# Optimization experiments

Measured on AMD Instinct MI355X. Metric: run time of the kernel, lower is better.

Reference implementation:

```python
import jax, jax.numpy as jnp
import numpy as np

EPS = 1e-10
ENTROPY_COEF = 0.1
COLSUM_COEF = 1.0


def setup_inputs() -> dict:
    key = jax.random.key(0)
    k1, k2, k3 = jax.random.split(key, 3)
    H, T, B, S = 512, 50003, 32, 256
    colsum_threshold = 0.5
    return {
        "text_input": jax.random.randint(k1, (B, S), 0, T, dtype=jnp.int32),
        "init_logits": jnp.zeros((H,), dtype=jnp.float32),
        "transition_logits": jax.random.normal(k2, (H, H), dtype=jnp.float32) * 0.1,
        "emission_logits": jax.random.normal(k3, (H, T), dtype=jnp.float32) * 0.1,
        "colsum_threshold": colsum_threshold,
    }


def reference(text_input, init_logits, transition_logits, emission_logits, colsum_threshold):
    # softmax-normalized HMM parameters
    text_pi = jax.nn.softmax(init_logits, axis=0)              # [H]
    text_A = jax.nn.softmax(transition_logits, axis=1)         # [H,H]
    text_B = jax.nn.softmax(emission_logits, axis=1)           # [H,T]

    log_pi = jnp.log(text_pi + EPS)                            # [H]
    log_A = jnpp = jnp.log(text_A + EPS)                       # [H,H]
    log_B = jnp.log(text_B + EPS)                              # [H,T]

    # gather per-token emission log-probs: [B,S,H]
    log_B_obs = log_B.T[text_input]

    # t = 0
    log_alpha0 = log_pi[None, :] + log_B_obs[:, 0, :]          # [B,H]

    def step(log_alpha, obs_t):
        # logsumexp over source state i: [B,H(i),1] + [1,H(i),H(j)] -> [B,H(j)]
        trans = log_alpha[:, :, None] + log_A[None, :, :]
        new_alpha = jax.nn.logsumexp(trans, axis=1) + obs_t
        return new_alpha, None

    obs_rest = jnp.swapaxes(log_B_obs[:, 1:, :], 0, 1)         # [S-1,B,H]
    log_alpha_final, _ = jax.lax.scan(step, log_alpha0, obs_rest)

    log_likelihood = jax.nn.logsumexp(log_alpha_final, axis=1)  # [B]
    likelihood_loss = -jnp.mean(log_likelihood)

    transition_entropy = -jnp.sum(text_A * jnp.log(text_A + EPS), axis=1)
    transition_entropy_loss = jnp.mean(transition_entropy) * ENTROPY_COEF

    col_sums = jnp.sum(text_A, axis=0)
    colsum_reg = jnp.sum(jax.nn.relu(colsum_threshold - col_sums)) * COLSUM_COEF

    hmm_loss = likelihood_loss + transition_entropy_loss + colsum_reg
    return text_pi, text_A, text_B, hmm_loss
```

## Files before the change

### kernel.cpp

```cpp
#include <hip/hip_runtime.h>
#include <hip/hip_bf16.h>
#include <stdint.h>

#define HH 512
#define BB 32
#define SSEQ 256
#define TVOC 50003
#define EPSF 1e-10f
#define EMSCALE 96.0f
#define TOTLOG 2759.2459164008406f

typedef float f32x4 __attribute__((ext_vector_type(4)));
typedef int v8i __attribute__((ext_vector_type(8)));

__device__ __forceinline__ float wave_max(float v) {
#pragma unroll
  for (int off = 32; off; off >>= 1) v = fmaxf(v, __shfl_xor(v, off));
  return v;
}
__device__ __forceinline__ float wave_sum(float v) {
#pragma unroll
  for (int off = 32; off; off >>= 1) v += __shfl_xor(v, off);
  return v;
}

__global__ __launch_bounds__(512) void init_ws_kernel(float* ws) {
  if (threadIdx.x < 8) ws[threadIdx.x] = 0.0f;
  ws[8 + threadIdx.x] = 0.0f;
}

__global__ __launch_bounds__(512) void softmax_pi_kernel(
    const float* __restrict__ x, float* __restrict__ pi) {
  const int tid = threadIdx.x;
  const int wv = tid >> 6, ln = tid & 63;
  __shared__ float red[8];
  float v = x[tid];
  float m = wave_max(v);
  if (ln == 0) red[wv] = m;
  __syncthreads();
  float M = red[0];
#pragma unroll
  for (int i = 1; i < 8; ++i) M = fmaxf(M, red[i]);
  float e = __expf(v - M);
  float s = wave_sum(e);
  __syncthreads();
  if (ln == 0) red[wv] = s;
  __syncthreads();
  float S = 0.f;
#pragma unroll
  for (int i = 0; i < 8; ++i) S += red[i];
  pi[tid] = e / S;
}

__global__ __launch_bounds__(512) void softmaxA_kernel(
    const float* __restrict__ tl, float* __restrict__ outA,
    float* __restrict__ ws_ent) {
  const int r = blockIdx.x, tid = threadIdx.x;
  const int wv = tid >> 6, ln = tid & 63;
  __shared__ float red[8];
  float v = tl[(size_t)r * HH + tid];
  float m = wave_max(v);
  if (ln == 0) red[wv] = m;
  __syncthreads();
  float M = red[0];
#pragma unroll
  for (int i = 1; i < 8; ++i) M = fmaxf(M, red[i]);
  float e = __expf(v - M);
  float s = wave_sum(e);
  __syncthreads();
  if (ln == 0) red[wv] = s;
  __syncthreads();
  float S = 0.f;
#pragma unroll
  for (int i = 0; i < 8; ++i) S += red[i];
  float p = e / S;
  outA[(size_t)r * HH + tid] = p;
  float ent = -p * __logf(p + EPSF);
  ent = wave_sum(ent);
  __syncthreads();
  if (ln == 0) red[wv] = ent;
  __syncthreads();
  if (tid == 0) {
    float tot = 0.f;
#pragma unroll
    for (int i = 0; i < 8; ++i) tot += red[i];
    atomicAdd(ws_ent, tot);
  }
}

__global__ __launch_bounds__(512) void colsum_partial_kernel(
    const float* __restrict__ outA, float* __restrict__ col) {
  const int j = threadIdx.x;
  const int i0 = blockIdx.x * 64;
  float s = 0.f;
#pragma unroll 4
  for (int i = i0; i < i0 + 64; ++i) s += outA[(size_t)i * HH + j];
  atomicAdd(&col[j], s);
}

__global__ __launch_bounds__(1024) void softmaxB_gather_kernel(
    const float* __restrict__ el, float* __restrict__ outB,
    const int* __restrict__ tok, __hip_bfloat16* __restrict__ ems) {
  const int r = blockIdx.x, tid = threadIdx.x;
  const float* x = el + (size_t)r * TVOC;
  float* yo = outB + (size_t)r * TVOC;
  const int mis = (int)(((16u - ((unsigned)(uintptr_t)x & 15u)) & 15u) >> 2);
  const int body = (TVOC - mis) >> 2;
  const int tailoff = mis + body * 4;

  float m = -1e30f, s = 0.f;
  auto upd = [&m, &s](float v) {
    if (v > m) { s = s * __expf(m - v) + 1.f; m = v; }
    else       { s += __expf(v - m); }
  };
  if (tid < mis) upd(x[tid]);
  const float4* x4 = (const float4*)(x + mis);
  for (int i = tid; i < body; i += 1024) {
    float4 v = x4[i];
    upd(v.x); upd(v.y); upd(v.z); upd(v.w);
  }
  for (int i = tailoff + tid; i < TVOC; i += 1024) upd(x[i]);

#pragma unroll
  for (int off = 32; off; off >>= 1) {
    float om = __shfl_down(m, off), os = __shfl_down(s, off);
    float nm = fmaxf(m, om);
    s = s * __expf(m - nm) + os * __expf(om - nm);
    m = nm;
  }
  __shared__ float sm[16], ssv[16];
  __shared__ float bM, biZ;
  if ((tid & 63) == 0) { sm[tid >> 6] = m; ssv[tid >> 6] = s; }
  __syncthreads();
  if (tid == 0) {
    float M = sm[0], S = ssv[0];
#pragma unroll
    for (int w = 1; w < 16; ++w) {
      float nm = fmaxf(M, sm[w]);
      S = S * __expf(M - nm) + ssv[w] * __expf(sm[w] - nm);
      M = nm;
    }
    bM = M; biZ = 1.f / S;
  }
  __syncthreads();
  const float M = bM, iZ = biZ;
  if (tid < mis) yo[tid] = __expf(x[tid] - M) * iZ;
  float4* y4 = (float4*)(yo + mis);
  for (int i = tid; i < body; i += 1024) {
    float4 v = x4[i];
    float4 o;
    o.x = __expf(v.x - M) * iZ;
    o.y = __expf(v.y - M) * iZ;
    o.z = __expf(v.z - M) * iZ;
    o.w = __expf(v.w - M) * iZ;
    y4[i] = o;
  }
  for (int i = tailoff + tid; i < TVOC; i += 1024)
    yo[i] = __expf(x[i] - M) * iZ;

  const float gs = EMSCALE * iZ;
  for (int idx = tid; idx < BB * SSEQ; idx += 1024) {
    const int sq = idx >> 5, b = idx & 31;
    const int t = tok[b * SSEQ + sq];
    ems[((size_t)sq * HH + r) * BB + b] = __float2bfloat16(__expf(x[t] - M) * gs);
  }
}

__global__ __launch_bounds__(1024) void scan_kernel(
    const float* __restrict__ d_pi, const float* __restrict__ d_A,
    const __hip_bfloat16* __restrict__ ems, float* __restrict__ ws_negll) {
  const int h = blockIdx.x;
  const int tid = threadIdx.x;
  const int lane = tid & 63;
  const int wave = tid >> 6;
  const int l15 = lane & 15;
  const int quad = lane >> 4;

  __shared__ __align__(16) unsigned char alpha[2][16][528];
  __shared__ float wmax[16][17];
  __shared__ float wsum[16][17];
  __shared__ float ls[16];

  const unsigned short* emsu = (const unsigned short*)ems;

  v8i aF[2][4];
#pragma unroll
  for (int n = 0; n < 2; ++n) {
    const int jg = wave * 32 + n * 16 + l15;
#pragma unroll
    for (int c = 0; c < 4; ++c) {
#pragma unroll
      for (int g = 0; g < 8; ++g) {
        const int k0 = c * 128 + quad * 32 + g * 4;
        const float v0 = d_A[(size_t)(k0 + 0) * HH + jg] * 512.0f;
        const float v1 = d_A[(size_t)(k0 + 1) * HH + jg] * 512.0f;
        const float v2 = d_A[(size_t)(k0 + 2) * HH + jg] * 512.0f;
        const float v3 = d_A[(size_t)(k0 + 3) * HH + jg] * 512.0f;
        int wrd = 0;
        wrd = __builtin_amdgcn_cvt_pk_fp8_f32(v0, v1, wrd, false);
        wrd = __builtin_amdgcn_cvt_pk_fp8_f32(v2, v3, wrd, true);
        aF[n][c][g] = wrd;
      }
    }
  }

  {
    const int b = wave;
    const int j0 = lane * 8;
    float vals[8];
    float m = -1e30f;
#pragma unroll
    for (int u = 0; u < 8; ++u) {
      const float e = __bfloat162float(ems[(size_t)(j0 + u) * BB + h * 16 + b]);
      vals[u] = (d_pi[j0 + u] + EPSF) * e;
      m = fmaxf(m, vals[u]);
    }
    m = wave_max(m);
    if (lane == 0) ls[b] = __logf(m);
    const float r = 1.0f / m;
    int lo = 0, hi = 0;
    lo = __builtin_amdgcn_cvt_pk_fp8_f32(vals[0] * r, vals[1] * r, lo, false);
    lo = __builtin_amdgcn_cvt_pk_fp8_f32(vals[2] * r, vals[3] * r, lo, true);
    hi = __builtin_amdgcn_cvt_pk_fp8_f32(vals[4] * r, vals[5] * r, hi, false);
    hi = __builtin_amdgcn_cvt_pk_fp8_f32(vals[6] * r, vals[7] * r, hi, true);
    *(unsigned int*)&alpha[0][b][j0]     = (unsigned)lo;
    *(unsigned int*)&alpha[0][b][j0 + 4] = (unsigned)hi;
  }
  __syncthreads();

  unsigned short evr[2][4];
#pragma unroll
  for (int n = 0; n < 2; ++n)
#pragma unroll
    for (int rg = 0; rg < 4; ++rg) {
      const int j = wave * 32 + n * 16 + quad * 4 + rg;
      evr[n][rg] = emsu[((size_t)1 * HH + j) * BB + h * 16 + l15];
    }

#pragma unroll 1
  for (int t = 1; t < SSEQ; ++t) {
    const int cur = (t - 1) & 1, nxt = t & 1;

    float ev[2][4];
#pragma unroll
    for (int n = 0; n < 2; ++n)
#pragma unroll
      for (int rg = 0; rg < 4; ++rg) {
        const unsigned u = (unsigned)evr[n][rg] << 16;
        ev[n][rg] = __uint_as_float(u);
      }
    const int tp = (t + 1 < SSEQ) ? t + 1 : SSEQ - 1;
#pragma unroll
    for (int n = 0; n < 2; ++n)
#pragma unroll
      for (int rg = 0; rg < 4; ++rg) {
        const int j = wave * 32 + n * 16 + quad * 4 + rg;
        evr[n][rg] = emsu[((size_t)tp * HH + j) * BB + h * 16 + l15];
      }

    f32x4 acc0 = {0.f, 0.f, 0.f, 0.f}, acc1 = {0.f, 0.f, 0.f, 0.f};
#pragma unroll
    for (int c = 0; c < 4; ++c) {
      const unsigned char* ap = &alpha[cur][l15][c * 128 + quad * 32];
      const int4 lo = *(const int4*)ap;
      const int4 hi = *(const int4*)(ap + 16);
      v8i bf;
      bf[0] = lo.x; bf[1] = lo.y; bf[2] = lo.z; bf[3] = lo.w;
      bf[4] = hi.x; bf[5] = hi.y; bf[6] = hi.z; bf[7] = hi.w;
      acc0 = __builtin_amdgcn_mfma_scale_f32_16x16x128_f8f6f4(
          aF[0][c], bf, acc0, 0, 0, 0, 0x7F7F7F7F, 0, 0x7F7F7F7F);
      acc1 = __builtin_amdgcn_mfma_scale_f32_16x16x128_f8f6f4(
          aF[1][c], bf, acc1, 0, 0, 0, 0x7F7F7F7F, 0, 0x7F7F7F7F);
    }

    float y[2][4];
#pragma unroll
    for (int rg = 0; rg < 4; ++rg) {
      y[0][rg] = acc0[rg] * ev[0][rg];
      y[1][rg] = acc1[rg] * ev[1][rg];
    }

    float r = 1.0f;
    if ((t & 15) == 0) {
      float mm = -1e30f;
#pragma unroll
      for (int rg = 0; rg < 4; ++rg)
        mm = fmaxf(mm, fmaxf(y[0][rg], y[1][rg]));
      mm = fmaxf(mm, __shfl_xor(mm, 16));
      mm = fmaxf(mm, __shfl_xor(mm, 32));
      if (lane < 16) wmax[wave][lane] = mm;
      __syncthreads();
      float m = wmax[0][l15];
#pragma unroll
      for (int w = 1; w < 16; ++w) m = fmaxf(m, wmax[w][l15]);
      r = 1.0f / m;
      if (tid < 16) ls[tid] += __logf(m);
    }

#pragma unroll
    for (int n = 0; n < 2; ++n) {
      int d = 0;
      d = __builtin_amdgcn_cvt_pk_fp8_f32(y[n][0] * r, y[n][1] * r, d, false);
      d = __builtin_amdgcn_cvt_pk_fp8_f32(y[n][2] * r, y[n][3] * r, d, true);
      *(unsigned int*)&alpha[nxt][l15][wave * 32 + n * 16 + quad * 4] = (unsigned)d;
    }
    if (t == SSEQ - 1) {
      float s = (y[0][0] + y[0][1] + y[0][2] + y[0][3] +
                 y[1][0] + y[1][1] + y[1][2] + y[1][3]) * r;
      s += __shfl_xor(s, 16);
      s += __shfl_xor(s, 32);
      if (lane < 16) wsum[wave][lane] = s;
    }
    __syncthreads();
  }

  if (wave == 0 && lane < 16) {
    float s = 0.f;
#pragma unroll
    for (int w = 0; w < 16; ++w) s += wsum[w][lane];
    const float LL = __logf(s) + ls[lane] - TOTLOG;
    atomicAdd(ws_negll, -LL * (1.0f / 32.0f));
  }
}

__global__ __launch_bounds__(512) void finalize_kernel(
    const float* __restrict__ ws, const float* __restrict__ col,
    const float* __restrict__ thr, float* __restrict__ out_loss) {
  const int j = threadIdx.x;
  float v = fmaxf(thr[0] - col[j], 0.f);
  v = wave_sum(v);
  __shared__ float red[8];
  if ((j & 63) == 0) red[j >> 6] = v;
  __syncthreads();
  if (j == 0) {
    float creg = 0.f;
#pragma unroll
    for (int i = 0; i < 8; ++i) creg += red[i];
    out_loss[0] = ws[1] + ws[0] * (0.1f / 512.0f) + creg;
  }
}

extern "C" void kernel_launch(void* const* d_in, const int* in_sizes, int n_in,
                              void* d_out, int out_size, void* d_ws, size_t ws_size,
                              hipStream_t stream) {
  const int*   tok    = (const int*)d_in[0];
  const float* initl  = (const float*)d_in[1];
  const float* transl = (const float*)d_in[2];
  const float* eml    = (const float*)d_in[3];
  const float* thr    = (const float*)d_in[4];

  float* out      = (float*)d_out;
  float* out_pi   = out;
  float* out_A    = out + HH;
  float* out_B    = out + HH + (size_t)HH * HH;
  float* out_loss = out + HH + (size_t)HH * HH + (size_t)HH * TVOC;

  float* wsf = (float*)d_ws;
  float* col = wsf + 8;
  __hip_bfloat16* ems = (__hip_bfloat16*)((char*)d_ws + 4096);

  init_ws_kernel<<<1, 512, 0, stream>>>(wsf);
  softmax_pi_kernel<<<1, 512, 0, stream>>>(initl, out_pi);
  softmaxA_kernel<<<512, 512, 0, stream>>>(transl, out_A, wsf + 0);
  colsum_partial_kernel<<<8, 512, 0, stream>>>(out_A, col);
  softmaxB_gather_kernel<<<512, 1024, 0, stream>>>(eml, out_B, tok, ems);
  scan_kernel<<<2, 1024, 0, stream>>>(out_pi, out_A, ems, wsf + 1);
  finalize_kernel<<<1, 512, 0, stream>>>(wsf, col, thr, out_loss);
}
```

Measured before the change: 598.1 us.

## Halve scan block to 8 waves with 64 output columns each; widen colsum grid

The scan kernel now runs 512 threads (8 waves) per block, and each wave computes four 16-column MFMA tiles instead of two. This keeps twice as much of the fp8 transition matrix in registers per wave and halves the number of waves taking part in each per-step barrier. The aim is to cut barrier and cross-wave synchronisation cost on the serial 255-step recurrence, at the price of more work per wave and higher register pressure. Separately, the colsum kernel is split across 32 blocks of 16 rows instead of 8 blocks of 64.

```diff
diff --git a/kernel.cpp b/kernel.cpp
--- a/kernel.cpp
+++ b/kernel.cpp
@@ -91,10 +91,10 @@
 __global__ __launch_bounds__(512) void colsum_partial_kernel(
     const float* __restrict__ outA, float* __restrict__ col) {
   const int j = threadIdx.x;
-  const int i0 = blockIdx.x * 64;
+  const int i0 = blockIdx.x * 16;
   float s = 0.f;
 #pragma unroll 4
-  for (int i = i0; i < i0 + 64; ++i) s += outA[(size_t)i * HH + j];
+  for (int i = i0; i < i0 + 16; ++i) s += outA[(size_t)i * HH + j];
   atomicAdd(&col[j], s);
 }
 
@@ -166,7 +166,7 @@
   }
 }
 
-__global__ __launch_bounds__(1024) void scan_kernel(
+__global__ __launch_bounds__(512, 2) void scan_kernel(
     const float* __restrict__ d_pi, const float* __restrict__ d_A,
     const __hip_bfloat16* __restrict__ ems, float* __restrict__ ws_negll) {
   const int h = blockIdx.x;
@@ -177,16 +177,16 @@
   const int quad = lane >> 4;
 
   __shared__ __align__(16) unsigned char alpha[2][16][528];
-  __shared__ float wmax[16][17];
-  __shared__ float wsum[16][17];
+  __shared__ float wmax[8][17];
+  __shared__ float wsum[8][17];
   __shared__ float ls[16];
 
   const unsigned short* emsu = (const unsigned short*)ems;
 
-  v8i aF[2][4];
-#pragma unroll
-  for (int n = 0; n < 2; ++n) {
-    const int jg = wave * 32 + n * 16 + l15;
+  v8i aF[4][4];
+#pragma unroll
+  for (int n = 0; n < 4; ++n) {
+    const int jg = wave * 64 + n * 16 + l15;
 #pragma unroll
     for (int c = 0; c < 4; ++c) {
 #pragma unroll
@@ -205,35 +205,37 @@
   }
 
   {
-    const int b = wave;
-    const int j0 = lane * 8;
-    float vals[8];
+    const int b = wave * 2 + (lane >> 5);
+    const int lh = lane & 31;
+    const int j0 = lh * 16;
+    float vals[16];
     float m = -1e30f;
 #pragma unroll
-    for (int u = 0; u < 8; ++u) {
+    for (int u = 0; u < 16; ++u) {
       const float e = __bfloat162float(ems[(size_t)(j0 + u) * BB + h * 16 + b]);
       vals[u] = (d_pi[j0 + u] + EPSF) * e;
       m = fmaxf(m, vals[u]);
     }
-    m = wave_max(m);
-    if (lane == 0) ls[b] = __logf(m);
+#pragma unroll
+    for (int off = 16; off; off >>= 1) m = fmaxf(m, __shfl_xor(m, off));
+    if (lh == 0) ls[b] = __logf(m);
     const float r = 1.0f / m;
-    int lo = 0, hi = 0;
-    lo = __builtin_amdgcn_cvt_pk_fp8_f32(vals[0] * r, vals[1] * r, lo, false);
-    lo = __builtin_amdgcn_cvt_pk_fp8_f32(vals[2] * r, vals[3] * r, lo, true);
-    hi = __builtin_amdgcn_cvt_pk_fp8_f32(vals[4] * r, vals[5] * r, hi, false);
-    hi = __builtin_amdgcn_cvt_pk_fp8_f32(vals[6] * r, vals[7] * r, hi, true);
-    *(unsigned int*)&alpha[0][b][j0]     = (unsigned)lo;
-    *(unsigned int*)&alpha[0][b][j0 + 4] = (unsigned)hi;
-  }
-  __syncthreads();
-
-  unsigned short evr[2][4];
-#pragma unroll
-  for (int n = 0; n < 2; ++n)
+#pragma unroll
+    for (int d = 0; d < 4; ++d) {
+      int wrd = 0;
+      wrd = __builtin_amdgcn_cvt_pk_fp8_f32(vals[d*4+0] * r, vals[d*4+1] * r, wrd, false);
+      wrd = __builtin_amdgcn_cvt_pk_fp8_f32(vals[d*4+2] * r, vals[d*4+3] * r, wrd, true);
+      *(unsigned int*)&alpha[0][b][j0 + d * 4] = (unsigned)wrd;
+    }
+  }
+  __syncthreads();
+
+  unsigned short evr[4][4];
+#pragma unroll
+  for (int n = 0; n < 4; ++n)
 #pragma unroll
     for (int rg = 0; rg < 4; ++rg) {
-      const int j = wave * 32 + n * 16 + quad * 4 + rg;
+      const int j = wave * 64 + n * 16 + quad * 4 + rg;
       evr[n][rg] = emsu[((size_t)1 * HH + j) * BB + h * 16 + l15];
     }
 
@@ -241,24 +243,24 @@
   for (int t = 1; t < SSEQ; ++t) {
     const int cur = (t - 1) & 1, nxt = t & 1;
 
-    float ev[2][4];
-#pragma unroll
-    for (int n = 0; n < 2; ++n)
-#pragma unroll
-      for (int rg = 0; rg < 4; ++rg) {
-        const unsigned u = (unsigned)evr[n][rg] << 16;
-        ev[n][rg] = __uint_as_float(u);
-      }
+    float ev[4][4];
+#pragma unroll
+    for (int n = 0; n < 4; ++n)
+#pragma unroll
+      for (int rg = 0; rg < 4; ++rg)
+        ev[n][rg] = __uint_as_float((unsigned)evr[n][rg] << 16);
+
     const int tp = (t + 1 < SSEQ) ? t + 1 : SSEQ - 1;
-#pragma unroll
-    for (int n = 0; n < 2; ++n)
-#pragma unroll
-      for (int rg = 0; rg < 4; ++rg) {
-        const int j = wave * 32 + n * 16 + quad * 4 + rg;
-        evr[n][rg] = emsu[((size_t)tp * HH + j) * BB + h * 16 + l15];
-      }
-
-    f32x4 acc0 = {0.f, 0.f, 0.f, 0.f}, acc1 = {0.f, 0.f, 0.f, 0.f};
+    const unsigned short* ep =
+        emsu + ((size_t)tp * HH + wave * 64 + quad * 4) * BB + h * 16 + l15;
+#pragma unroll
+    for (int n = 0; n < 4; ++n)
+#pragma unroll
+      for (int rg = 0; rg < 4; ++rg)
+        evr[n][rg] = ep[(n * 16 + rg) * BB];
+
+    f32x4 acc[4] = {{0.f,0.f,0.f,0.f},{0.f,0.f,0.f,0.f},
+                    {0.f,0.f,0.f,0.f},{0.f,0.f,0.f,0.f}};
 #pragma unroll
     for (int c = 0; c < 4; ++c) {
       const unsigned char* ap = &alpha[cur][l15][c * 128 + quad * 32];
@@ -267,46 +269,50 @@
       v8i bf;
       bf[0] = lo.x; bf[1] = lo.y; bf[2] = lo.z; bf[3] = lo.w;
       bf[4] = hi.x; bf[5] = hi.y; bf[6] = hi.z; bf[7] = hi.w;
-      acc0 = __builtin_amdgcn_mfma_scale_f32_16x16x128_f8f6f4(
-          aF[0][c], bf, acc0, 0, 0, 0, 0x7F7F7F7F, 0, 0x7F7F7F7F);
-      acc1 = __builtin_amdgcn_mfma_scale_f32_16x16x128_f8f6f4(
-          aF[1][c], bf, acc1, 0, 0, 0, 0x7F7F7F7F, 0, 0x7F7F7F7F);
-    }
-
-    float y[2][4];
-#pragma unroll
-    for (int rg = 0; rg < 4; ++rg) {
-      y[0][rg] = acc0[rg] * ev[0][rg];
-      y[1][rg] = acc1[rg] * ev[1][rg];
-    }
+#pragma unroll
+      for (int n = 0; n < 4; ++n)
+        acc[n] = __builtin_amdgcn_mfma_scale_f32_16x16x128_f8f6f4(
+            aF[n][c], bf, acc[n], 0, 0, 0, 0x7F7F7F7F, 0, 0x7F7F7F7F);
+    }
+
+    float y[4][4];
+#pragma unroll
+    for (int n = 0; n < 4; ++n)
+#pragma unroll
+      for (int rg = 0; rg < 4; ++rg)
+        y[n][rg] = acc[n][rg] * ev[n][rg];
 
     float r = 1.0f;
     if ((t & 15) == 0) {
       float mm = -1e30f;
 #pragma unroll
-      for (int rg = 0; rg < 4; ++rg)
-        mm = fmaxf(mm, fmaxf(y[0][rg], y[1][rg]));
+      for (int n = 0; n < 4; ++n)
+#pragma unroll
+        for (int rg = 0; rg < 4; ++rg) mm = fmaxf(mm, y[n][rg]);
       mm = fmaxf(mm, __shfl_xor(mm, 16));
       mm = fmaxf(mm, __shfl_xor(mm, 32));
       if (lane < 16) wmax[wave][lane] = mm;
       __syncthreads();
       float m = wmax[0][l15];
 #pragma unroll
-      for (int w = 1; w < 16; ++w) m = fmaxf(m, wmax[w][l15]);
+      for (int w = 1; w < 8; ++w) m = fmaxf(m, wmax[w][l15]);
       r = 1.0f / m;
       if (tid < 16) ls[tid] += __logf(m);
     }
 
 #pragma unroll
-    for (int n = 0; n < 2; ++n) {
+    for (int n = 0; n < 4; ++n) {
       int d = 0;
       d = __builtin_amdgcn_cvt_pk_fp8_f32(y[n][0] * r, y[n][1] * r, d, false);
       d = __builtin_amdgcn_cvt_pk_fp8_f32(y[n][2] * r, y[n][3] * r, d, true);
-      *(unsigned int*)&alpha[nxt][l15][wave * 32 + n * 16 + quad * 4] = (unsigned)d;
+      *(unsigned int*)&alpha[nxt][l15][wave * 64 + n * 16 + quad * 4] = (unsigned)d;
     }
     if (t == SSEQ - 1) {
-      float s = (y[0][0] + y[0][1] + y[0][2] + y[0][3] +
-                 y[1][0] + y[1][1] + y[1][2] + y[1][3]) * r;
+      float s = 0.f;
+#pragma unroll
+      for (int n = 0; n < 4; ++n)
+        s += y[n][0] + y[n][1] + y[n][2] + y[n][3];
+      s *= r;
       s += __shfl_xor(s, 16);
       s += __shfl_xor(s, 32);
       if (lane < 16) wsum[wave][lane] = s;
@@ -317,7 +323,7 @@
   if (wave == 0 && lane < 16) {
     float s = 0.f;
 #pragma unroll
-    for (int w = 0; w < 16; ++w) s += wsum[w][lane];
+    for (int w = 0; w < 8; ++w) s += wsum[w][lane];
     const float LL = __logf(s) + ls[lane] - TOTLOG;
     atomicAdd(ws_negll, -LL * (1.0f / 32.0f));
   }
@@ -362,8 +368,8 @@
   init_ws_kernel<<<1, 512, 0, stream>>>(wsf);
   softmax_pi_kernel<<<1, 512, 0, stream>>>(initl, out_pi);
   softmaxA_kernel<<<512, 512, 0, stream>>>(transl, out_A, wsf + 0);
-  colsum_partial_kernel<<<8, 512, 0, stream>>>(out_A, col);
+  colsum_partial_kernel<<<32, 512, 0, stream>>>(out_A, col);
   softmaxB_gather_kernel<<<512, 1024, 0, stream>>>(eml, out_B, tok, ems);
-  scan_kernel<<<2, 1024, 0, stream>>>(out_pi, out_A, ems, wsf + 1);
+  scan_kernel<<<2, 512, 0, stream>>>(out_pi, out_A, ems, wsf + 1);
   finalize_kernel<<<1, 512, 0, stream>>>(wsf, col, thr, out_loss);
 }
```

New measurement: 633.7 us. 5.9% more time.
